# Optimization experiments

Measured on AMD Instinct MI355X. Metric: run time of the kernel, lower is better.

Reference implementation:

```python
import jax, jax.numpy as jnp
import numpy as np

B, N, U = 4, 4096, 512


def setup_inputs() -> dict:
    key = jax.random.key(0)
    ks = jax.random.split(key, 5)
    s = 1.0 / np.sqrt(U)
    return {
        "x": jax.random.normal(ks[0], (B, N, U), dtype=jnp.float32),
        "Wq": jax.random.normal(ks[1], (U, U), dtype=jnp.float32) * s,
        "bq": jnp.zeros((U,), dtype=jnp.float32),
        "Wk": jax.random.normal(ks[2], (U, U), dtype=jnp.float32) * s,
        "bk": jnp.zeros((U,), dtype=jnp.float32),
        "Wv": jax.random.normal(ks[3], (U, U), dtype=jnp.float32) * s,
        "bv": jnp.zeros((U,), dtype=jnp.float32),
        "Wp": jax.random.normal(ks[4], (U, U), dtype=jnp.float32) * s,
        "bp": jnp.zeros((U,), dtype=jnp.float32),
    }


def reference(x, Wq, bq, Wk, bk, Wv, bv, Wp, bp):
    # x: [B, N, U] single-head self-attention with residual
    scale = jnp.asarray(x.shape[-1], jnp.float32) ** -0.5
    q = x @ Wq + bq
    k = x @ Wk + bk
    v = x @ Wv + bv
    scores = jnp.einsum("bnd,bmd->bnm", q, k) * scale  # [B, N, N]
    attn = jax.nn.softmax(scores, axis=-1)
    ctx = jnp.einsum("bnm,bmd->bnd", attn, v)
    return x + (ctx @ Wp + bp)
```

## Files before the change

### kernel.cpp

```cpp
#include <hip/hip_runtime.h>
#include <hip/hip_bf16.h>
#include <math.h>

#define NB 4
#define NN 4096
#define UU 512

using short8  = __attribute__((ext_vector_type(8))) short;
using bf16x8  = __attribute__((ext_vector_type(8))) __bf16;
using floatx4 = __attribute__((ext_vector_type(4))) float;

__device__ __forceinline__ floatx4 mfma16(short8 a, short8 b, floatx4 c) {
    return __builtin_amdgcn_mfma_f32_16x16x32_bf16(
        __builtin_bit_cast(bf16x8, a), __builtin_bit_cast(bf16x8, b), c, 0, 0, 0);
}

__device__ __forceinline__ unsigned short f2bf(float f) {
    union { float f; unsigned u; } v; v.f = f;
    return (unsigned short)((v.u + 0x7fffu + ((v.u >> 16) & 1u)) >> 16);
}
__device__ __forceinline__ float bf2f(unsigned short s) {
    union { unsigned u; float f; } v; v.u = ((unsigned)s) << 16; return v.f;
}

#define GLL16(gp, lp) __builtin_amdgcn_global_load_lds( \
    (const __attribute__((address_space(1))) void*)(gp), \
    (__attribute__((address_space(3))) void*)(lp), 16, 0, 0)

__global__ void __launch_bounds__(256) k_cvt_x(const float* __restrict__ x,
                                               unsigned short* __restrict__ xb) {
    int i = (blockIdx.x * 256 + threadIdx.x) * 4;
    float4 v = *(const float4*)(x + i);
    ushort4 o;
    o.x = f2bf(v.x); o.y = f2bf(v.y); o.z = f2bf(v.z); o.w = f2bf(v.w);
    *(ushort4*)(xb + i) = o;
}

__global__ void __launch_bounds__(256) k_cvt_w(const float* __restrict__ W,
                                               unsigned short* __restrict__ WT) {
    int idx = blockIdx.x * 256 + threadIdx.x;
    int n = idx >> 9, k = idx & 511;
    WT[idx] = f2bf(W[k * 512 + n]);
}

__global__ void __launch_bounds__(256, 2) k_proj(
    const unsigned short* __restrict__ Xb,
    const unsigned short* __restrict__ WqT, const unsigned short* __restrict__ WkT,
    const unsigned short* __restrict__ WvT,
    const float* __restrict__ bq, const float* __restrict__ bk, const float* __restrict__ bv,
    unsigned short* __restrict__ Q, unsigned short* __restrict__ K8,
    unsigned short* __restrict__ V8)
{
    __shared__ __align__(16) unsigned short As[128 * 32];
    __shared__ __align__(16) unsigned short Bs[128 * 32];
    const int z = blockIdx.z;
    const unsigned short* WT = (z == 0) ? WqT : (z == 1) ? WkT : WvT;
    const float* bias = (z == 0) ? bq : (z == 1) ? bk : bv;
    const int t = threadIdx.x, wave = t >> 6, lane = t & 63;
    const int quad = lane >> 4, l16 = lane & 15;
    const int m0 = blockIdx.x * 128, n0 = blockIdx.y * 128;
    const int wm = wave >> 1, wn = wave & 1;

    const int srow = wave * 32 + (lane >> 2);
    const int scol = (lane & 3) * 8;
    const unsigned short* gA = Xb + (size_t)(m0 + srow) * UU + scol;
    const unsigned short* gB = WT + (size_t)(n0 + srow) * UU + scol;
    unsigned short* lA = As + wave * 1024;
    unsigned short* lB = Bs + wave * 1024;

    floatx4 acc[4][4] = {};

    for (int k0 = 0; k0 < UU; k0 += 32) {
        GLL16(gA + k0, lA);
        GLL16(gA + k0 + 16 * UU, lA + 512);
        GLL16(gB + k0, lB);
        GLL16(gB + k0 + 16 * UU, lB + 512);
        __syncthreads();
        short8 a[4], b[4];
        #pragma unroll
        for (int i = 0; i < 4; i++)
            a[i] = *(const short8*)(As + (wm * 64 + i * 16 + l16) * 32 + quad * 8);
        #pragma unroll
        for (int j = 0; j < 4; j++)
            b[j] = *(const short8*)(Bs + (wn * 64 + j * 16 + l16) * 32 + quad * 8);
        #pragma unroll
        for (int i = 0; i < 4; i++)
            #pragma unroll
            for (int j = 0; j < 4; j++)
                acc[i][j] = mfma16(a[i], b[j], acc[i][j]);
        __syncthreads();
    }

    #pragma unroll
    for (int j = 0; j < 4; j++) {
        const int n = n0 + wn * 64 + j * 16 + l16;
        const float bv_ = bias[n];
        #pragma unroll
        for (int i = 0; i < 4; i++) {
            const int mb = m0 + wm * 64 + i * 16 + quad * 4;
            const int bb = mb >> 12, tok = mb & (NN - 1);
            if (z == 0) {
                #pragma unroll
                for (int r = 0; r < 4; r++)
                    Q[(size_t)(mb + r) * UU + n] = f2bf(acc[i][j][r] + bv_);
            } else if (z == 1) {
                const size_t base = (size_t)bb * NN * UU + (size_t)(n >> 3) * (NN * 8)
                                  + (size_t)tok * 8 + (n & 7);
                #pragma unroll
                for (int r = 0; r < 4; r++)
                    K8[base + (size_t)r * 8] = f2bf(acc[i][j][r] + bv_);
            } else {
                ushort4 o;
                o.x = f2bf(acc[i][j][0] + bv_);
                o.y = f2bf(acc[i][j][1] + bv_);
                o.z = f2bf(acc[i][j][2] + bv_);
                o.w = f2bf(acc[i][j][3] + bv_);
                *(ushort4*)(V8 + (size_t)bb * NN * UU + (size_t)(tok >> 3) * (UU * 8)
                            + (size_t)n * 8 + (tok & 7)) = o;
            }
        }
    }
}

__global__ void __launch_bounds__(512, 1) k_flash(
    const unsigned short* __restrict__ Q,
    const unsigned short* __restrict__ K8,
    const unsigned short* __restrict__ V8,
    unsigned short* __restrict__ ctx)
{
    __shared__ __align__(16) unsigned short Ks[64 * 64 * 8];
    __shared__ __align__(16) unsigned short Vs[8 * 512 * 8];
    __shared__ __align__(16) float S_lds[64 * 68];
    __shared__ __align__(16) unsigned short P_lds[64 * 72];
    __shared__ float m_lds[64], l_lds[64], a_lds[64];

    const int b = blockIdx.y;
    const int q0 = blockIdx.x * 64;
    const int t = threadIdx.x;
    const int wave = t >> 6, lane = t & 63, quad = lane >> 4, l16 = lane & 15;
    const int qt = wave >> 1;
    const int kh = wave & 1;
    const int dh = wave & 1;

    if (t < 64) { m_lds[t] = -INFINITY; l_lds[t] = 0.f; }

    const unsigned short* qp = Q + (size_t)(b * NN + q0 + qt * 16 + l16) * UU + quad * 8;
    short8 qf[16];
    #pragma unroll
    for (int kk = 0; kk < 16; kk++) qf[kk] = *(const short8*)(qp + kk * 32);

    const unsigned short* K8b = K8 + (size_t)b * NN * UU;
    const unsigned short* V8b = V8 + (size_t)b * NN * UU;

    #pragma unroll
    for (int j = 0; j < 8; j++) {
        const int dc = wave * 8 + j;
        GLL16(K8b + (size_t)dc * (NN * 8) + lane * 8, Ks + dc * 512 + lane * 8);
    }

    floatx4 o[16] = {};
    const float sscale = 0.04419417382415922f * 1.4426950408889634f;

    __syncthreads();

    for (int kt = 0; kt < NN; kt += 64) {
        #pragma unroll
        for (int j = 0; j < 8; j++) {
            const int c = wave * 8 + j;
            GLL16(V8b + (size_t)kt * 512 + (size_t)c * 512 + lane * 8, Vs + c * 512 + lane * 8);
        }

        floatx4 s0 = {}, s1 = {};
        #pragma unroll
        for (int kk = 0; kk < 16; kk++) {
            const unsigned short* kb = Ks + (kk * 4 + quad) * 512 + (kh * 32 + l16) * 8;
            short8 b0 = *(const short8*)(kb);
            short8 b1 = *(const short8*)(kb + 128);
            s0 = mfma16(qf[kk], b0, s0);
            s1 = mfma16(qf[kk], b1, s1);
        }
        #pragma unroll
        for (int i = 0; i < 4; i++) {
            S_lds[(qt * 16 + quad * 4 + i) * 68 + kh * 32 + l16]      = s0[i] * sscale;
            S_lds[(qt * 16 + quad * 4 + i) * 68 + kh * 32 + 16 + l16] = s1[i] * sscale;
        }
        __syncthreads();

        {
            const int row = t >> 3, c8 = (t & 7) * 8;
            const float4* sp = (const float4*)(S_lds + row * 68 + c8);
            float4 va = sp[0], vb = sp[1];
            float mx = fmaxf(fmaxf(fmaxf(va.x, va.y), fmaxf(va.z, va.w)),
                             fmaxf(fmaxf(vb.x, vb.y), fmaxf(vb.z, vb.w)));
            mx = fmaxf(mx, __shfl_xor(mx, 1, 8));
            mx = fmaxf(mx, __shfl_xor(mx, 2, 8));
            mx = fmaxf(mx, __shfl_xor(mx, 4, 8));
            const float m_old = m_lds[row];
            const float m_new = fmaxf(m_old, mx);
            float p[8] = { exp2f(va.x - m_new), exp2f(va.y - m_new),
                           exp2f(va.z - m_new), exp2f(va.w - m_new),
                           exp2f(vb.x - m_new), exp2f(vb.y - m_new),
                           exp2f(vb.z - m_new), exp2f(vb.w - m_new) };
            short8 pv; float sum = 0.f;
            #pragma unroll
            for (int j = 0; j < 8; j++) {
                unsigned short us = f2bf(p[j]);
                pv[j] = (short)us;
                sum += bf2f(us);
            }
            *(short8*)(P_lds + row * 72 + c8) = pv;
            sum += __shfl_xor(sum, 1, 8);
            sum += __shfl_xor(sum, 2, 8);
            sum += __shfl_xor(sum, 4, 8);
            if ((t & 7) == 0) {
                const float alpha = exp2f(m_old - m_new);
                a_lds[row] = alpha;
                m_lds[row] = m_new;
                l_lds[row] = l_lds[row] * alpha + sum;
            }
        }
        __syncthreads();

        if (kt + 64 < NN) {
            #pragma unroll
            for (int j = 0; j < 8; j++) {
                const int dc = wave * 8 + j;
                GLL16(K8b + (size_t)dc * (NN * 8) + (size_t)(kt + 64 + lane) * 8,
                      Ks + dc * 512 + lane * 8);
            }
        }

        float al[4];
        #pragma unroll
        for (int i = 0; i < 4; i++) al[i] = a_lds[qt * 16 + quad * 4 + i];
        #pragma unroll
        for (int dt = 0; dt < 16; dt++)
            #pragma unroll
            for (int i = 0; i < 4; i++) o[dt][i] *= al[i];
        const short8 a0 = *(const short8*)(P_lds + (qt * 16 + l16) * 72 + quad * 8);
        const short8 a1 = *(const short8*)(P_lds + (qt * 16 + l16) * 72 + 32 + quad * 8);
        #pragma unroll
        for (int dt = 0; dt < 16; dt++) {
            const int d = dh * 256 + dt * 16 + l16;
            short8 b0 = *(const short8*)(Vs + quad * 4096 + d * 8);
            short8 b1 = *(const short8*)(Vs + (4 + quad) * 4096 + d * 8);
            o[dt] = mfma16(a0, b0, o[dt]);
            o[dt] = mfma16(a1, b1, o[dt]);
        }
        __syncthreads();
    }

    float linv[4];
    #pragma unroll
    for (int i = 0; i < 4; i++) linv[i] = 1.f / l_lds[qt * 16 + quad * 4 + i];
    #pragma unroll
    for (int dt = 0; dt < 16; dt++) {
        const int d = dh * 256 + dt * 16 + l16;
        #pragma unroll
        for (int i = 0; i < 4; i++)
            ctx[(size_t)(b * NN + q0 + qt * 16 + quad * 4 + i) * UU + d] = f2bf(o[dt][i] * linv[i]);
    }
}

__global__ void __launch_bounds__(256, 2) k_out(
    const unsigned short* __restrict__ Cx,
    const unsigned short* __restrict__ WpT,
    const float* __restrict__ bp,
    const float* __restrict__ x,
    float* __restrict__ out)
{
    __shared__ __align__(16) unsigned short As[128 * 32];
    __shared__ __align__(16) unsigned short Bs[128 * 32];
    const int t = threadIdx.x, wave = t >> 6, lane = t & 63;
    const int quad = lane >> 4, l16 = lane & 15;
    const int m0 = blockIdx.x * 128, n0 = blockIdx.y * 128;
    const int wm = wave >> 1, wn = wave & 1;
    const int srow = wave * 32 + (lane >> 2);
    const int scol = (lane & 3) * 8;
    const unsigned short* gA = Cx + (size_t)(m0 + srow) * UU + scol;
    const unsigned short* gB = WpT + (size_t)(n0 + srow) * UU + scol;
    unsigned short* lA = As + wave * 1024;
    unsigned short* lB = Bs + wave * 1024;

    floatx4 acc[4][4] = {};

    for (int k0 = 0; k0 < UU; k0 += 32) {
        GLL16(gA + k0, lA);
        GLL16(gA + k0 + 16 * UU, lA + 512);
        GLL16(gB + k0, lB);
        GLL16(gB + k0 + 16 * UU, lB + 512);
        __syncthreads();
        short8 a[4], b[4];
        #pragma unroll
        for (int i = 0; i < 4; i++)
            a[i] = *(const short8*)(As + (wm * 64 + i * 16 + l16) * 32 + quad * 8);
        #pragma unroll
        for (int j = 0; j < 4; j++)
            b[j] = *(const short8*)(Bs + (wn * 64 + j * 16 + l16) * 32 + quad * 8);
        #pragma unroll
        for (int i = 0; i < 4; i++)
            #pragma unroll
            for (int j = 0; j < 4; j++)
                acc[i][j] = mfma16(a[i], b[j], acc[i][j]);
        __syncthreads();
    }

    #pragma unroll
    for (int j = 0; j < 4; j++) {
        const int n = n0 + wn * 64 + j * 16 + l16;
        const float bv_ = bp[n];
        #pragma unroll
        for (int i = 0; i < 4; i++) {
            const int mb = m0 + wm * 64 + i * 16 + quad * 4;
            #pragma unroll
            for (int r = 0; r < 4; r++) {
                const size_t idx = (size_t)(mb + r) * UU + n;
                out[idx] = acc[i][j][r] + bv_ + x[idx];
            }
        }
    }
}

extern "C" void kernel_launch(void* const* d_in, const int* in_sizes, int n_in,
                              void* d_out, int out_size, void* d_ws, size_t ws_size,
                              hipStream_t stream)
{
    const float* x  = (const float*)d_in[0];
    const float* Wq = (const float*)d_in[1];
    const float* bq = (const float*)d_in[2];
    const float* Wk = (const float*)d_in[3];
    const float* bk = (const float*)d_in[4];
    const float* Wv = (const float*)d_in[5];
    const float* bv = (const float*)d_in[6];
    const float* Wp = (const float*)d_in[7];
    const float* bp = (const float*)d_in[8];
    float* out = (float*)d_out;

    char* ws = (char*)d_ws;
    unsigned short* Xb  = (unsigned short*)(ws);
    unsigned short* WqT = (unsigned short*)(ws + 16777216);
    unsigned short* WkT = (unsigned short*)(ws + 17301504);
    unsigned short* WvT = (unsigned short*)(ws + 17825792);
    unsigned short* WpT = (unsigned short*)(ws + 18350080);
    unsigned short* Qm  = (unsigned short*)(ws + 18874368);
    unsigned short* K8m = (unsigned short*)(ws + 35651584);
    unsigned short* V8m = (unsigned short*)(ws + 52428800);
    unsigned short* Cx  = (unsigned short*)(ws + 69206016);

    hipLaunchKernelGGL(k_cvt_x, dim3(8192), dim3(256), 0, stream, x, Xb);
    hipLaunchKernelGGL(k_cvt_w, dim3(1024), dim3(256), 0, stream, Wq, WqT);
    hipLaunchKernelGGL(k_cvt_w, dim3(1024), dim3(256), 0, stream, Wk, WkT);
    hipLaunchKernelGGL(k_cvt_w, dim3(1024), dim3(256), 0, stream, Wv, WvT);
    hipLaunchKernelGGL(k_cvt_w, dim3(1024), dim3(256), 0, stream, Wp, WpT);
    hipLaunchKernelGGL(k_proj, dim3(128, 4, 3), dim3(256), 0, stream,
                       Xb, WqT, WkT, WvT, bq, bk, bv, Qm, K8m, V8m);
    hipLaunchKernelGGL(k_flash, dim3(64, 4), dim3(512), 0, stream, Qm, K8m, V8m, Cx);
    hipLaunchKernelGGL(k_out, dim3(128, 4), dim3(256), 0, stream, Cx, WpT, bp, x, out);
}
```

Baseline: 371.4 us.

## Repartition flash-attention waves into 32x32 register tiles with split-K score reduction

Each wave now computes a 32-query by 32-key score tile over half of the head dimension, and a 32-query by 128-dim slice of the output, instead of 16-row strips. Each K/V fragment read from LDS is therefore reused by two MFMAs, which cuts LDS read traffic per MFMA. Because the QK^T reduction is split across two waves, partial scores are combined with LDS float atomicAdd, and S_lds is re-zeroed after every read. This adds atomic LDS traffic and an extra store per tile.

Measured after the change: 1.010 ms. 172% more time.

```diff
diff --git a/kernel.cpp b/kernel.cpp
--- a/kernel.cpp
+++ b/kernel.cpp
@@ -138,16 +138,26 @@
     const int q0 = blockIdx.x * 64;
     const int t = threadIdx.x;
     const int wave = t >> 6, lane = t & 63, quad = lane >> 4, l16 = lane & 15;
-    const int qt = wave >> 1;
-    const int kh = wave & 1;
+    const int qh = wave >> 2;
+    const int kh = (wave >> 1) & 1;
     const int dh = wave & 1;
+    const int dq = wave & 3;
 
     if (t < 64) { m_lds[t] = -INFINITY; l_lds[t] = 0.f; }
-
-    const unsigned short* qp = Q + (size_t)(b * NN + q0 + qt * 16 + l16) * UU + quad * 8;
-    short8 qf[16];
-    #pragma unroll
-    for (int kk = 0; kk < 16; kk++) qf[kk] = *(const short8*)(qp + kk * 32);
+    #pragma unroll
+    for (int i = 0; i < 3; i++) {
+        const int idx = t + i * 512;
+        if (idx < 64 * 17) ((float4*)S_lds)[idx] = make_float4(0.f, 0.f, 0.f, 0.f);
+    }
+
+    const unsigned short* qp = Q + (size_t)(b * NN + q0 + qh * 32 + l16) * UU
+                             + dh * 256 + quad * 8;
+    short8 qf[2][8];
+    #pragma unroll
+    for (int qi = 0; qi < 2; qi++)
+        #pragma unroll
+        for (int kk = 0; kk < 8; kk++)
+            qf[qi][kk] = *(const short8*)(qp + qi * 16 * UU + kk * 32);
 
     const unsigned short* K8b = K8 + (size_t)b * NN * UU;
     const unsigned short* V8b = V8 + (size_t)b * NN * UU;
@@ -158,7 +168,7 @@
         GLL16(K8b + (size_t)dc * (NN * 8) + lane * 8, Ks + dc * 512 + lane * 8);
     }
 
-    floatx4 o[16] = {};
+    floatx4 o[2][8] = {};
     const float sscale = 0.04419417382415922f * 1.4426950408889634f;
 
     __syncthreads();
@@ -170,26 +180,35 @@
             GLL16(V8b + (size_t)kt * 512 + (size_t)c * 512 + lane * 8, Vs + c * 512 + lane * 8);
         }
 
-        floatx4 s0 = {}, s1 = {};
-        #pragma unroll
-        for (int kk = 0; kk < 16; kk++) {
-            const unsigned short* kb = Ks + (kk * 4 + quad) * 512 + (kh * 32 + l16) * 8;
+        floatx4 sacc[2][2] = {};
+        #pragma unroll
+        for (int kk = 0; kk < 8; kk++) {
+            const unsigned short* kb = Ks + (size_t)(dh * 32 + kk * 4 + quad) * 512
+                                     + (kh * 32 + l16) * 8;
             short8 b0 = *(const short8*)(kb);
             short8 b1 = *(const short8*)(kb + 128);
-            s0 = mfma16(qf[kk], b0, s0);
-            s1 = mfma16(qf[kk], b1, s1);
-        }
-        #pragma unroll
-        for (int i = 0; i < 4; i++) {
-            S_lds[(qt * 16 + quad * 4 + i) * 68 + kh * 32 + l16]      = s0[i] * sscale;
-            S_lds[(qt * 16 + quad * 4 + i) * 68 + kh * 32 + 16 + l16] = s1[i] * sscale;
-        }
+            sacc[0][0] = mfma16(qf[0][kk], b0, sacc[0][0]);
+            sacc[1][0] = mfma16(qf[1][kk], b0, sacc[1][0]);
+            sacc[0][1] = mfma16(qf[0][kk], b1, sacc[0][1]);
+            sacc[1][1] = mfma16(qf[1][kk], b1, sacc[1][1]);
+        }
+        #pragma unroll
+        for (int qi = 0; qi < 2; qi++)
+            #pragma unroll
+            for (int kj = 0; kj < 2; kj++)
+                #pragma unroll
+                for (int r = 0; r < 4; r++)
+                    atomicAdd(&S_lds[(qh * 32 + qi * 16 + quad * 4 + r) * 68
+                                     + kh * 32 + kj * 16 + l16],
+                              sacc[qi][kj][r] * sscale);
         __syncthreads();
 
         {
             const int row = t >> 3, c8 = (t & 7) * 8;
-            const float4* sp = (const float4*)(S_lds + row * 68 + c8);
+            float4* sp = (float4*)(S_lds + row * 68 + c8);
             float4 va = sp[0], vb = sp[1];
+            sp[0] = make_float4(0.f, 0.f, 0.f, 0.f);
+            sp[1] = make_float4(0.f, 0.f, 0.f, 0.f);
             float mx = fmaxf(fmaxf(fmaxf(va.x, va.y), fmaxf(va.z, va.w)),
                              fmaxf(fmaxf(vb.x, vb.y), fmaxf(vb.z, vb.w)));
             mx = fmaxf(mx, __shfl_xor(mx, 1, 8));
@@ -230,36 +249,56 @@
             }
         }
 
-        float al[4];
-        #pragma unroll
-        for (int i = 0; i < 4; i++) al[i] = a_lds[qt * 16 + quad * 4 + i];
-        #pragma unroll
-        for (int dt = 0; dt < 16; dt++)
-            #pragma unroll
-            for (int i = 0; i < 4; i++) o[dt][i] *= al[i];
-        const short8 a0 = *(const short8*)(P_lds + (qt * 16 + l16) * 72 + quad * 8);
-        const short8 a1 = *(const short8*)(P_lds + (qt * 16 + l16) * 72 + 32 + quad * 8);
-        #pragma unroll
-        for (int dt = 0; dt < 16; dt++) {
-            const int d = dh * 256 + dt * 16 + l16;
-            short8 b0 = *(const short8*)(Vs + quad * 4096 + d * 8);
-            short8 b1 = *(const short8*)(Vs + (4 + quad) * 4096 + d * 8);
-            o[dt] = mfma16(a0, b0, o[dt]);
-            o[dt] = mfma16(a1, b1, o[dt]);
-        }
-        __syncthreads();
-    }
-
-    float linv[4];
-    #pragma unroll
-    for (int i = 0; i < 4; i++) linv[i] = 1.f / l_lds[qt * 16 + quad * 4 + i];
-    #pragma unroll
-    for (int dt = 0; dt < 16; dt++) {
-        const int d = dh * 256 + dt * 16 + l16;
-        #pragma unroll
-        for (int i = 0; i < 4; i++)
-            ctx[(size_t)(b * NN + q0 + qt * 16 + quad * 4 + i) * UU + d] = f2bf(o[dt][i] * linv[i]);
-    }
+        float al[2][4];
+        #pragma unroll
+        for (int qi = 0; qi < 2; qi++)
+            #pragma unroll
+            for (int i = 0; i < 4; i++)
+                al[qi][i] = a_lds[qh * 32 + qi * 16 + quad * 4 + i];
+        #pragma unroll
+        for (int qi = 0; qi < 2; qi++)
+            #pragma unroll
+            for (int dt = 0; dt < 8; dt++)
+                #pragma unroll
+                for (int i = 0; i < 4; i++)
+                    o[qi][dt][i] *= al[qi][i];
+
+        short8 aP[2][2];
+        #pragma unroll
+        for (int qi = 0; qi < 2; qi++)
+            #pragma unroll
+            for (int kk = 0; kk < 2; kk++)
+                aP[qi][kk] = *(const short8*)(P_lds + (qh * 32 + qi * 16 + l16) * 72
+                                              + kk * 32 + quad * 8);
+        #pragma unroll
+        for (int dt = 0; dt < 8; dt++) {
+            const int d = dq * 128 + dt * 16 + l16;
+            short8 v0 = *(const short8*)(Vs + quad * 4096 + d * 8);
+            short8 v1 = *(const short8*)(Vs + (4 + quad) * 4096 + d * 8);
+            o[0][dt] = mfma16(aP[0][0], v0, o[0][dt]);
+            o[1][dt] = mfma16(aP[1][0], v0, o[1][dt]);
+            o[0][dt] = mfma16(aP[0][1], v1, o[0][dt]);
+            o[1][dt] = mfma16(aP[1][1], v1, o[1][dt]);
+        }
+        __syncthreads();
+    }
+
+    float linv[2][4];
+    #pragma unroll
+    for (int qi = 0; qi < 2; qi++)
+        #pragma unroll
+        for (int i = 0; i < 4; i++)
+            linv[qi][i] = 1.f / l_lds[qh * 32 + qi * 16 + quad * 4 + i];
+    #pragma unroll
+    for (int qi = 0; qi < 2; qi++)
+        #pragma unroll
+        for (int dt = 0; dt < 8; dt++) {
+            const int d = dq * 128 + dt * 16 + l16;
+            #pragma unroll
+            for (int i = 0; i < 4; i++)
+                ctx[(size_t)(b * NN + q0 + qh * 32 + qi * 16 + quad * 4 + i) * UU + d]
+                    = f2bf(o[qi][dt][i] * linv[qi][i]);
+        }
 }
 
 __global__ void __launch_bounds__(256, 2) k_out(
```
